# Kernel tuning notes

Measured on AMD Instinct MI355X. Metric: run time of the kernel, lower is better.

The kernel has to match this reference:

```python
import jax, jax.numpy as jnp
import numpy as np

N_CLASSES = 2048
NUM_GROUP = 8
CLS_PER_GROUP = N_CLASSES // NUM_GROUP  # 256
NUM_SAMPLE = 10
EMB_DIM = 400
COMMITMENT = 0.25


def setup_inputs() -> dict:
    key = jax.random.key(0)
    k1, k2 = jax.random.split(key)
    x0 = jax.random.normal(k1, (64, 512, 1, EMB_DIM), dtype=jnp.float32)
    emb = jax.random.normal(k2, (N_CLASSES, EMB_DIM), dtype=jnp.float32)
    return {"x0": x0, "emb": emb}


def reference(x0, emb):
    x = x0  # normalize=False path
    M = x0.shape[0] * x0.shape[1] * x0.shape[2]
    x1 = x.reshape(M, EMB_DIM)

    # pairwise squared distances [M, N_CLASSES]
    d = (jnp.sum(x1 ** 2, axis=1, keepdims=True)
         + jnp.sum(emb ** 2, axis=1)
         - 2.0 * x1 @ emb.T)

    # per-group mean distance -> group argmin
    d_g = d.reshape(M, NUM_GROUP, CLS_PER_GROUP)
    group = jnp.argmin(jnp.mean(d_g, axis=2), axis=1)  # [M]

    # inverse-distance probs restricted to the chosen group
    d_sel = jnp.take_along_axis(d_g, group[:, None, None], axis=1)[:, 0, :]  # [M, CLS_PER_GROUP]
    prob_sel = 1.0 / d_sel
    p, idx_local = jax.lax.top_k(prob_sel, NUM_SAMPLE)  # descending, [M, NUM_SAMPLE]
    index = group[:, None] * CLS_PER_GROUP + idx_local  # global codebook indices

    # L1 normalize kept probabilities (F.normalize p=1)
    prob_dist = p / jnp.maximum(jnp.sum(jnp.abs(p), axis=1, keepdims=True), 1e-12)

    # entropy of top-1 code histogram
    hist = jnp.bincount(index[:, 0], length=N_CLASSES).astype(jnp.float32)
    pr = hist / jnp.float32(M)
    entropy = -jnp.sum(jnp.where(hist > 0, pr * jnp.log(jnp.where(hist > 0, pr, 1.0)), 0.0))

    # weighted gather-sum of code vectors (probs are detached in original)
    gathered = emb[index]  # [M, NUM_SAMPLE, EMB_DIM]
    w = jax.lax.stop_gradient(prob_dist)[:, :, None]
    output = jnp.sum(gathered * w, axis=1).reshape(x.shape)

    out0 = jax.lax.stop_gradient(output - x) + x  # straight-through
    q_latent = jnp.mean((jax.lax.stop_gradient(x) - output) ** 2)
    e_latent = jnp.mean((x - jax.lax.stop_gradient(output)) ** 2)
    loss = q_latent + COMMITMENT * e_latent

    encodings = (1.0 / d)[None]  # [1, M, N_CLASSES]
    return (loss, out0, entropy, encodings)
```

## Files before the change

### kernel.cpp

```cpp
#include <hip/hip_runtime.h>
#include <math.h>

#define M_ROWS 32768
#define N_CLS  2048
#define NGRP   8
#define CPG    256
#define NS     10
#define NCAND  16
#define EDIM   400
#define KPAD   416
#define NKT    13
#define BK     32
#define SGS    448
#define NPART  32

typedef _Float16 f16x8 __attribute__((ext_vector_type(8)));
typedef float f32x4 __attribute__((ext_vector_type(4)));

__device__ __forceinline__ void gld_lds16(const void* g, void* l) {
    __builtin_amdgcn_global_load_lds(
        (const __attribute__((address_space(1))) unsigned int*)g,
        (__attribute__((address_space(3))) unsigned int*)l, 16, 0, 0);
}

__global__ __launch_bounds__(256) void k_split_hi(const float* __restrict__ in,
                                                  unsigned short* __restrict__ hi,
                                                  float* __restrict__ ss, int rows) {
    int row  = blockIdx.x * 4 + (threadIdx.x >> 6);
    int lane = threadIdx.x & 63;
    if (row >= rows) return;
    const float* src = in + (size_t)row * EDIM;
    unsigned short* ph = hi + (size_t)row * KPAD;
    float s = 0.f;
    #pragma unroll
    for (int q = 0; q < 2; ++q) {
        int c4 = lane + q * 64;
        if (c4 < KPAD / 4) {
            int k = c4 * 4;
            float4 v = make_float4(0.f, 0.f, 0.f, 0.f);
            if (k < EDIM) v = *(const float4*)(src + k);
            float va[4] = {v.x, v.y, v.z, v.w};
            unsigned short ha[4];
            #pragma unroll
            for (int t = 0; t < 4; ++t) {
                float f = va[t];
                _Float16 h = (_Float16)f;
                ha[t] = __builtin_bit_cast(unsigned short, h);
                s = fmaf(f, f, s);
            }
            ushort4 H; H.x = ha[0]; H.y = ha[1]; H.z = ha[2]; H.w = ha[3];
            *(ushort4*)(ph + k) = H;
        }
    }
    #pragma unroll
    for (int o = 32; o; o >>= 1) s += __shfl_xor(s, o, 64);
    if (lane == 0) ss[row] = s;
}

__global__ __launch_bounds__(448) void k_groupsum(const float* __restrict__ emb,
                                                  const unsigned short* __restrict__ ehi,
                                                  float* __restrict__ Sg,
                                                  float* __restrict__ SgH) {
    const int g = blockIdx.x;
    const int t = threadIdx.x;
    float se = 0.f, sh = 0.f;
    if (t < EDIM) {
        for (int j = 0; j < CPG; ++j) {
            se += emb[(size_t)(g * CPG + j) * EDIM + t];
            _Float16 h = __builtin_bit_cast(_Float16, ehi[(size_t)(g * CPG + j) * KPAD + t]);
            sh += (float)h;
        }
    }
    Sg[g * SGS + t]  = se;
    SgH[g * SGS + t] = sh;
}

__global__ __launch_bounds__(256, 4) void k_dist1(
    const unsigned short* __restrict__ xhi, const unsigned short* __restrict__ ehi,
    const float* __restrict__ xx, const float* __restrict__ ee,
    float* __restrict__ enc, float* __restrict__ gsum) {
    __shared__ __attribute__((aligned(16))) _Float16 Ah[128][BK];
    __shared__ __attribute__((aligned(16))) _Float16 Bh[128][BK];

    const int wg    = blockIdx.x;
    const int xcd   = wg & 7;
    const int local = wg >> 3;
    const int mx    = xcd * 32 + (local & 31);
    const int ny    = local >> 5;
    const int m0    = mx * 128;
    const int n0    = ny * 128;

    const int tid  = threadIdx.x;
    const int lane = tid & 63, wid = tid >> 6;
    const int wr = (wid >> 1) * 64, wc = (wid & 1) * 64;
    const int lr = lane & 15, ko = lane >> 4;

    f32x4 acc[4][4];
    #pragma unroll
    for (int i = 0; i < 4; ++i)
        #pragma unroll
        for (int j = 0; j < 4; ++j) { f32x4 z = {0.f, 0.f, 0.f, 0.f}; acc[i][j] = z; }

    for (int kt = 0; kt < NKT; ++kt) {
        const int k0 = kt * BK;
        #pragma unroll
        for (int q = 0; q < 2; ++q) {
            int c = q * 256 + tid;
            int row = c >> 2, kc = c & 3;
            size_t goA = (size_t)(m0 + row) * KPAD + k0 + kc * 8;
            size_t goB = (size_t)(n0 + row) * KPAD + k0 + kc * 8;
            int loff = (c >> 6) * 1024;
            gld_lds16(xhi + goA, (char*)&Ah[0][0] + loff);
            gld_lds16(ehi + goB, (char*)&Bh[0][0] + loff);
        }
        __syncthreads();

        f16x8 a_h[4];
        #pragma unroll
        for (int i = 0; i < 4; ++i)
            a_h[i] = *(const f16x8*)&Ah[wr + i * 16 + lr][ko * 8];
        #pragma unroll
        for (int j = 0; j < 4; ++j) {
            f16x8 b_h = *(const f16x8*)&Bh[wc + j * 16 + lr][ko * 8];
            #pragma unroll
            for (int i = 0; i < 4; ++i)
                acc[i][j] = __builtin_amdgcn_mfma_f32_16x16x32_f16(a_h[i], b_h, acc[i][j], 0, 0, 0);
        }
        __syncthreads();
    }

    #pragma unroll
    for (int i = 0; i < 4; ++i) {
        #pragma unroll
        for (int r = 0; r < 4; ++r) {
            int row = m0 + wr + i * 16 + ko * 4 + r;
            float xm = xx[row];
            float rs = 0.f;
            #pragma unroll
            for (int j = 0; j < 4; ++j) {
                int col = n0 + wc + j * 16 + lr;
                float dd = fmaf(-2.f, acc[i][j][r], xm + ee[col]);
                rs += dd;
                enc[(size_t)row * N_CLS + col] = 1.0f / dd;
            }
            rs += __shfl_xor(rs, 1, 64);
            rs += __shfl_xor(rs, 2, 64);
            rs += __shfl_xor(rs, 4, 64);
            rs += __shfl_xor(rs, 8, 64);
            if (lr == 0)
                gsum[(size_t)row * NPART + ny * 2 + (wc >> 6)] = rs;
        }
    }
}

__global__ __launch_bounds__(256) void k_select3(const float* __restrict__ x,
                                                 const float* __restrict__ emb,
                                                 const float* __restrict__ enc,
                                                 const float* __restrict__ gsum,
                                                 const float* __restrict__ Sg,
                                                 const float* __restrict__ SgH,
                                                 const float* __restrict__ xx,
                                                 const float* __restrict__ ee,
                                                 float* __restrict__ out0,
                                                 float* __restrict__ rmse,
                                                 unsigned int* __restrict__ hist) {
    __shared__ __attribute__((aligned(16))) float xs[4][EDIM];

    const int wave = threadIdx.x >> 6;
    const int lane = threadIdx.x & 63;
    const int m = blockIdx.x * 4 + wave;

    const float* xrg = x + (size_t)m * EDIM;
    float xr[7], xh[7];
    #pragma unroll
    for (int k = 0; k < 7; ++k) {
        int d = lane + 64 * k;
        float f = (d < EDIM) ? xrg[d] : 0.f;
        xr[k] = f;
        xh[k] = (float)(_Float16)f;
        if (d < EDIM) xs[wave][d] = f;
    }
    const float xm = xx[m];

    float aD[NGRP];
    #pragma unroll
    for (int g = 0; g < NGRP; ++g) aD[g] = 0.f;
    #pragma unroll
    for (int k = 0; k < 7; ++k) {
        int d = lane + 64 * k;
        #pragma unroll
        for (int g = 0; g < NGRP; ++g) {
            aD[g] = fmaf(xr[k], Sg[g * SGS + d], aD[g]);
            aD[g] = fmaf(-xh[k], SgH[g * SGS + d], aD[g]);
        }
    }
    const float* gs = gsum + (size_t)m * NPART;
    int bestg = 0; float bestv = 0.f;
    #pragma unroll
    for (int g = 0; g < NGRP; ++g) {
        float sD = aD[g];
        #pragma unroll
        for (int o = 1; o < 64; o <<= 1) sD += __shfl_xor(sD, o, 64);
        float base = 0.f;
        #pragma unroll
        for (int p = 0; p < 4; ++p) base += gs[g * 4 + p];
        float sc = fmaf(-2.f, sD, base);
        if (g == 0 || sc < bestv) { bestv = sc; bestg = g; }
    }
    const int j0 = bestg * CPG;

    const float* pr = enc + (size_t)m * N_CLS + j0;
    float v0 = pr[lane], v1 = pr[lane + 64], v2 = pr[lane + 128], v3 = pr[lane + 192];

    int cand = 0;
    #pragma unroll
    for (int t = 0; t < NCAND; ++t) {
        float bv = v0; int bs = 0;
        if (v1 > bv) { bv = v1; bs = 1; }
        if (v2 > bv) { bv = v2; bs = 2; }
        if (v3 > bv) { bv = v3; bs = 3; }
        int bidx = lane + 64 * bs;
        #pragma unroll
        for (int o = 1; o < 64; o <<= 1) {
            float ov = __shfl_xor(bv, o, 64);
            int   oi = __shfl_xor(bidx, o, 64);
            if (ov > bv || (ov == bv && oi < bidx)) { bv = ov; bidx = oi; }
        }
        if (lane == t) cand = bidx;
        bool me = (bidx & 63) == lane;
        int  sl = bidx >> 6;
        v0 = (me && sl == 0) ? -INFINITY : v0;
        v1 = (me && sl == 1) ? -INFINITY : v1;
        v2 = (me && sl == 2) ? -INFINITY : v2;
        v3 = (me && sl == 3) ? -INFINITY : v3;
    }

    int cj = __shfl(cand, lane >> 2, 64);
    int jg = j0 + cj;
    const float4* er4 = (const float4*)(emb + (size_t)jg * EDIM);
    const float4* xs4 = (const float4*)(&xs[wave][0]);
    float a = 0.f;
    #pragma unroll
    for (int q = 0; q < 25; ++q) {
        int idx = (lane & 3) + 4 * q;
        float4 e = er4[idx];
        float4 xv = xs4[idx];
        a = fmaf(xv.x, e.x, a);
        a = fmaf(xv.y, e.y, a);
        a = fmaf(xv.z, e.z, a);
        a = fmaf(xv.w, e.w, a);
    }
    a += __shfl_xor(a, 1, 64);
    a += __shfl_xor(a, 2, 64);
    float dd = fmaf(-2.f, a, xm + ee[jg]);
    float pvq = 1.0f / dd;
    float pcur = __shfl(pvq, (lane & 15) * 4, 64);
    if (lane >= NCAND) pcur = -INFINITY;
    int ccur = cand;

    float wsel = 0.f; int gsel = 0;
    #pragma unroll
    for (int t = 0; t < NS; ++t) {
        float bv = pcur; int bc = ccur; int bl = lane;
        #pragma unroll
        for (int o = 1; o < 16; o <<= 1) {
            float ov = __shfl_xor(bv, o, 64);
            int   oc = __shfl_xor(bc, o, 64);
            int   ol = __shfl_xor(bl, o, 64);
            if (ov > bv || (ov == bv && oc < bc)) { bv = ov; bc = oc; bl = ol; }
        }
        if (lane == bl) pcur = -INFINITY;
        if (lane == t) { wsel = bv; gsel = j0 + bc; }
    }

    float ps = (lane < NS) ? fabsf(wsel) : 0.f;
    #pragma unroll
    for (int o = 1; o < 16; o <<= 1) ps += __shfl_xor(ps, o, 64);
    float wn = fmaxf(__shfl(ps, 0, 64), 1e-12f);

    if (lane == 0) atomicAdd(&hist[gsel], 1u);

    float wt[NS]; int gt[NS];
    #pragma unroll
    for (int t = 0; t < NS; ++t) {
        wt[t] = __shfl(wsel, t, 64) / wn;
        gt[t] = __shfl(gsel, t, 64);
    }
    float* orow = out0 + (size_t)m * EDIM;
    float sq = 0.f;
    #pragma unroll
    for (int k = 0; k < 7; ++k) {
        int d = lane + 64 * k;
        if (d < EDIM) {
            float o = 0.f;
            #pragma unroll
            for (int t = 0; t < NS; ++t) o = fmaf(wt[t], emb[(size_t)gt[t] * EDIM + d], o);
            float xv = xr[k];
            float diff = xv - o;
            sq = fmaf(diff, diff, sq);
            orow[d] = (o - xv) + xv;
        }
    }
    #pragma unroll
    for (int o = 32; o; o >>= 1) sq += __shfl_xor(sq, o, 64);
    if (lane == 0) rmse[m] = sq;
}

__global__ __launch_bounds__(1024) void k_final(const float* __restrict__ rmse,
                                                const unsigned int* __restrict__ hist,
                                                float* __restrict__ loss_out,
                                                float* __restrict__ ent_out) {
    __shared__ float red[1024];
    const int t = threadIdx.x;

    float s = 0.f;
    for (int i = t; i < M_ROWS; i += 1024) s += rmse[i];
    red[t] = s; __syncthreads();
    for (int off = 512; off; off >>= 1) {
        if (t < off) red[t] += red[t + off];
        __syncthreads();
    }
    if (t == 0) {
        float q = red[0] / 13107200.0f;
        loss_out[0] = q + 0.25f * q;
    }
    __syncthreads();

    float e = 0.f;
    for (int i = t; i < N_CLS; i += 1024) {
        unsigned int h = hist[i];
        if (h > 0) {
            float prb = (float)h / 32768.0f;
            e -= prb * logf(prb);
        }
    }
    red[t] = e; __syncthreads();
    for (int off = 512; off; off >>= 1) {
        if (t < off) red[t] += red[t + off];
        __syncthreads();
    }
    if (t == 0) ent_out[0] = red[0];
}

extern "C" void kernel_launch(void* const* d_in, const int* in_sizes, int n_in,
                              void* d_out, int out_size, void* d_ws, size_t ws_size,
                              hipStream_t stream) {
    const float* x   = (const float*)d_in[0];
    const float* emb = (const float*)d_in[1];

    float* out      = (float*)d_out;
    float* loss_out = out;
    float* out0     = out + 1;
    float* ent_out  = out + 1 + M_ROWS * EDIM;
    float* enc      = out + 2 + M_ROWS * EDIM;

    float* ws   = (float*)d_ws;
    float* ee   = ws;
    float* xx   = ee + N_CLS;
    float* Sg   = xx + M_ROWS;
    float* SgH  = Sg + NGRP * SGS;
    float* gsum = SgH + NGRP * SGS;
    float* rmse = gsum + (size_t)M_ROWS * NPART;
    unsigned int* hist = (unsigned int*)(rmse + M_ROWS);
    float* fend = rmse + M_ROWS + N_CLS;

    unsigned short* xhi = (unsigned short*)fend;
    unsigned short* ehi = xhi + (size_t)M_ROWS * KPAD;

    hipMemsetAsync(hist, 0, N_CLS * sizeof(unsigned int), stream);

    k_split_hi<<<M_ROWS / 4, 256, 0, stream>>>(x, xhi, xx, M_ROWS);
    k_split_hi<<<N_CLS / 4, 256, 0, stream>>>(emb, ehi, ee, N_CLS);
    k_groupsum<<<NGRP, 448, 0, stream>>>(emb, ehi, Sg, SgH);

    k_dist1<<<(M_ROWS / 128) * (N_CLS / 128), 256, 0, stream>>>(xhi, ehi, xx, ee, enc, gsum);

    k_select3<<<M_ROWS / 4, 256, 0, stream>>>(x, emb, enc, gsum, Sg, SgH, xx, ee,
                                              out0, rmse, hist);

    k_final<<<1, 1024, 0, stream>>>(rmse, hist, loss_out, ent_out);
}
```

Measured before the change: 400.7 us.

## Streamline select kernel with packed-key candidate search and bitonic top-k sort

Rewrites the per-row selection kernel. Group reduction now uses a transposed butterfly so each lane group ends up with one group's sum, instead of eight full wave reductions. Candidate extraction packs each probability and its index into one unsigned key, so the search needs a single shuffle per step instead of value plus index. The final top-10 is a 16-lane bitonic sort rather than ten repeated argmax passes, and the x row is read from global memory instead of shared memory. Masking the low 8 mantissa bits changes tie handling and can reorder candidates whose values are nearly equal. The packed key also assumes positive probabilities.

```diff
diff --git a/kernel.cpp b/kernel.cpp
--- a/kernel.cpp
+++ b/kernel.cpp
@@ -153,7 +153,7 @@
     }
 }
 
-__global__ __launch_bounds__(256) void k_select3(const float* __restrict__ x,
+__global__ __launch_bounds__(256) void k_select4(const float* __restrict__ x,
                                                  const float* __restrict__ emb,
                                                  const float* __restrict__ enc,
                                                  const float* __restrict__ gsum,
@@ -164,8 +164,6 @@
                                                  float* __restrict__ out0,
                                                  float* __restrict__ rmse,
                                                  unsigned int* __restrict__ hist) {
-    __shared__ __attribute__((aligned(16))) float xs[4][EDIM];
-
     const int wave = threadIdx.x >> 6;
     const int lane = threadIdx.x & 63;
     const int m = blockIdx.x * 4 + wave;
@@ -178,7 +176,6 @@
         float f = (d < EDIM) ? xrg[d] : 0.f;
         xr[k] = f;
         xh[k] = (float)(_Float16)f;
-        if (d < EDIM) xs[wave][d] = f;
     }
     const float xm = xx[m];
 
@@ -194,51 +191,70 @@
             aD[g] = fmaf(-xh[k], SgH[g * SGS + d], aD[g]);
         }
     }
+    #pragma unroll
+    for (int g = 0; g < NGRP; ++g) {
+        aD[g] += __shfl_xor(aD[g], 8, 64);
+        aD[g] += __shfl_xor(aD[g], 16, 64);
+        aD[g] += __shfl_xor(aD[g], 32, 64);
+    }
+    const int myg = (lane >> 3) & 7;
+    float s = aD[0];
+    s = (myg == 1) ? aD[1] : s;
+    s = (myg == 2) ? aD[2] : s;
+    s = (myg == 3) ? aD[3] : s;
+    s = (myg == 4) ? aD[4] : s;
+    s = (myg == 5) ? aD[5] : s;
+    s = (myg == 6) ? aD[6] : s;
+    s = (myg == 7) ? aD[7] : s;
+    s += __shfl_xor(s, 1, 64);
+    s += __shfl_xor(s, 2, 64);
+    s += __shfl_xor(s, 4, 64);
     const float* gs = gsum + (size_t)m * NPART;
-    int bestg = 0; float bestv = 0.f;
-    #pragma unroll
-    for (int g = 0; g < NGRP; ++g) {
-        float sD = aD[g];
-        #pragma unroll
-        for (int o = 1; o < 64; o <<= 1) sD += __shfl_xor(sD, o, 64);
-        float base = 0.f;
-        #pragma unroll
-        for (int p = 0; p < 4; ++p) base += gs[g * 4 + p];
-        float sc = fmaf(-2.f, sD, base);
-        if (g == 0 || sc < bestv) { bestv = sc; bestg = g; }
-    }
-    const int j0 = bestg * CPG;
+    float base = gs[myg * 4 + 0] + gs[myg * 4 + 1] + gs[myg * 4 + 2] + gs[myg * 4 + 3];
+    float sc = fmaf(-2.f, s, base);
+    int bg = myg; float bv = sc;
+    #pragma unroll
+    for (int o = 8; o < 64; o <<= 1) {
+        float ov = __shfl_xor(bv, o, 64);
+        int   og = __shfl_xor(bg, o, 64);
+        if (ov < bv || (ov == bv && og < bg)) { bv = ov; bg = og; }
+    }
+    const int j0 = bg * CPG;
 
     const float* pr = enc + (size_t)m * N_CLS + j0;
-    float v0 = pr[lane], v1 = pr[lane + 64], v2 = pr[lane + 128], v3 = pr[lane + 192];
-
-    int cand = 0;
+    float4 pv4 = *(const float4*)(pr + lane * 4);
+    unsigned key0 = (__float_as_uint(pv4.x) & 0xFFFFFF00u) | (255u - (unsigned)(lane * 4 + 0));
+    unsigned key1 = (__float_as_uint(pv4.y) & 0xFFFFFF00u) | (255u - (unsigned)(lane * 4 + 1));
+    unsigned key2 = (__float_as_uint(pv4.z) & 0xFFFFFF00u) | (255u - (unsigned)(lane * 4 + 2));
+    unsigned key3 = (__float_as_uint(pv4.w) & 0xFFFFFF00u) | (255u - (unsigned)(lane * 4 + 3));
+
+    unsigned candKey = 0;
     #pragma unroll
     for (int t = 0; t < NCAND; ++t) {
-        float bv = v0; int bs = 0;
-        if (v1 > bv) { bv = v1; bs = 1; }
-        if (v2 > bv) { bv = v2; bs = 2; }
-        if (v3 > bv) { bv = v3; bs = 3; }
-        int bidx = lane + 64 * bs;
+        unsigned a01 = key0 > key1 ? key0 : key1;
+        unsigned a23 = key2 > key3 ? key2 : key3;
+        unsigned mk  = a01 > a23 ? a01 : a23;
         #pragma unroll
         for (int o = 1; o < 64; o <<= 1) {
-            float ov = __shfl_xor(bv, o, 64);
-            int   oi = __shfl_xor(bidx, o, 64);
-            if (ov > bv || (ov == bv && oi < bidx)) { bv = ov; bidx = oi; }
-        }
-        if (lane == t) cand = bidx;
-        bool me = (bidx & 63) == lane;
-        int  sl = bidx >> 6;
-        v0 = (me && sl == 0) ? -INFINITY : v0;
-        v1 = (me && sl == 1) ? -INFINITY : v1;
-        v2 = (me && sl == 2) ? -INFINITY : v2;
-        v3 = (me && sl == 3) ? -INFINITY : v3;
-    }
+            unsigned ok = (unsigned)__shfl_xor((int)mk, o, 64);
+            mk = ok > mk ? ok : mk;
+        }
+        if (lane == t) candKey = mk;
+        unsigned widx = 255u - (mk & 0xFFu);
+        if ((widx >> 2) == (unsigned)lane) {
+            unsigned slot = widx & 3u;
+            key0 = (slot == 0u) ? 0u : key0;
+            key1 = (slot == 1u) ? 0u : key1;
+            key2 = (slot == 2u) ? 0u : key2;
+            key3 = (slot == 3u) ? 0u : key3;
+        }
+    }
+    int cand = 255 - (int)(candKey & 0xFFu);
 
     int cj = __shfl(cand, lane >> 2, 64);
     int jg = j0 + cj;
     const float4* er4 = (const float4*)(emb + (size_t)jg * EDIM);
-    const float4* xs4 = (const float4*)(&xs[wave][0]);
+    const float4* xs4 = (const float4*)xrg;
     float a = 0.f;
     #pragma unroll
     for (int q = 0; q < 25; ++q) {
@@ -255,36 +271,37 @@
     float dd = fmaf(-2.f, a, xm + ee[jg]);
     float pvq = 1.0f / dd;
     float pcur = __shfl(pvq, (lane & 15) * 4, 64);
-    if (lane >= NCAND) pcur = -INFINITY;
-    int ccur = cand;
-
-    float wsel = 0.f; int gsel = 0;
+    int   ccur = __shfl(cand, lane & 15, 64);
+
+    const int l16 = lane & 15;
+    #pragma unroll
+    for (int k = 2; k <= 16; k <<= 1) {
+        #pragma unroll
+        for (int j = k >> 1; j > 0; j >>= 1) {
+            float opv = __shfl_xor(pcur, j, 16);
+            int   occ = __shfl_xor(ccur, j, 16);
+            bool amLow     = (l16 & j) == 0;
+            bool blockDesc = (l16 & k) == 0;
+            bool iGreater  = (pcur > opv) || (pcur == opv && ccur < occ);
+            bool keep = (amLow == blockDesc) ? iGreater : !iGreater;
+            if (!keep) { pcur = opv; ccur = occ; }
+        }
+    }
+
+    float ps = (l16 < NS) ? pcur : 0.f;
+    ps += __shfl_xor(ps, 1, 16);
+    ps += __shfl_xor(ps, 2, 16);
+    ps += __shfl_xor(ps, 4, 16);
+    ps += __shfl_xor(ps, 8, 16);
+    float wn = fmaxf(ps, 1e-12f);
+
+    if (lane == 0) atomicAdd(&hist[j0 + ccur], 1u);
+
+    float wt[NS]; int gt[NS];
     #pragma unroll
     for (int t = 0; t < NS; ++t) {
-        float bv = pcur; int bc = ccur; int bl = lane;
-        #pragma unroll
-        for (int o = 1; o < 16; o <<= 1) {
-            float ov = __shfl_xor(bv, o, 64);
-            int   oc = __shfl_xor(bc, o, 64);
-            int   ol = __shfl_xor(bl, o, 64);
-            if (ov > bv || (ov == bv && oc < bc)) { bv = ov; bc = oc; bl = ol; }
-        }
-        if (lane == bl) pcur = -INFINITY;
-        if (lane == t) { wsel = bv; gsel = j0 + bc; }
-    }
-
-    float ps = (lane < NS) ? fabsf(wsel) : 0.f;
-    #pragma unroll
-    for (int o = 1; o < 16; o <<= 1) ps += __shfl_xor(ps, o, 64);
-    float wn = fmaxf(__shfl(ps, 0, 64), 1e-12f);
-
-    if (lane == 0) atomicAdd(&hist[gsel], 1u);
-
-    float wt[NS]; int gt[NS];
-    #pragma unroll
-    for (int t = 0; t < NS; ++t) {
-        wt[t] = __shfl(wsel, t, 64) / wn;
-        gt[t] = __shfl(gsel, t, 64);
+        wt[t] = __shfl(pcur, t, 16) / wn;
+        gt[t] = j0 + __shfl(ccur, t, 16);
     }
     float* orow = out0 + (size_t)m * EDIM;
     float sq = 0.f;
@@ -375,7 +392,7 @@
 
     k_dist1<<<(M_ROWS / 128) * (N_CLS / 128), 256, 0, stream>>>(xhi, ehi, xx, ee, enc, gsum);
 
-    k_select3<<<M_ROWS / 4, 256, 0, stream>>>(x, emb, enc, gsum, Sg, SgH, xx, ee,
+    k_select4<<<M_ROWS / 4, 256, 0, stream>>>(x, emb, enc, gsum, Sg, SgH, xx, ee,
                                               out0, rmse, hist);
 
     k_final<<<1, 1024, 0, stream>>>(rmse, hist, loss_out, ent_out);
```

Result: faster. 360.0 us (-10.2%).
